# Kernel tuning notes

Measured on AMD Instinct MI355X. Metric: run time of the kernel, lower is better.

## Reference

```python
import jax, jax.numpy as jnp
import numpy as np

B, NLAT, NLON, V = 2, 181, 360, 78
NGRID = NLAT * NLON
NMESH, NEDGE = 10242, 163840
NODE_D, EDGE_D, HID, NLAYERS = 256, 64, 512, 16


def _mlp(x, w1, b1, w2, b2):
    # 2-layer MLP with ReLU (matches MLP(input_dim, hidden_dim, output_dim, n_layers=2))
    return jax.nn.relu(x @ w1 + b1) @ w2 + b2


def setup_inputs() -> dict:
    key = jax.random.key(0)
    ks = jax.random.split(key, 40)
    s = 0.02
    p = {}
    p["x_current"] = jax.random.normal(ks[0], (B, NLAT, NLON, V), jnp.float32)
    p["x_previous"] = jax.random.normal(ks[1], (B, NLAT, NLON, V), jnp.float32)
    p["mesh_node_feats"] = jax.random.normal(ks[2], (NMESH, 7), jnp.float32)
    p["raw_edge_feats"] = jax.random.normal(ks[3], (NEDGE, 4), jnp.float32)
    p["edge_index"] = jax.random.randint(ks[4], (2, NEDGE), 0, NMESH, jnp.int32)
    p["g2m_idx"] = jax.random.randint(ks[5], (NMESH,), 0, NGRID, jnp.int32)  # nearest grid point per mesh node
    p["m2g_idx"] = jax.random.randint(ks[6], (NGRID,), 0, NMESH, jnp.int32)  # nearest mesh node per grid point
    enc_in = 2 * V + 7  # grid channels (current||previous) + 7 mesh geometric features
    p["enc_w1"] = s * jax.random.normal(ks[7], (enc_in, HID), jnp.float32)
    p["enc_b1"] = jnp.zeros((HID,), jnp.float32)
    p["enc_w2"] = s * jax.random.normal(ks[8], (HID, NODE_D), jnp.float32)
    p["enc_b2"] = jnp.zeros((NODE_D,), jnp.float32)
    p["eme_w1"] = s * jax.random.normal(ks[9], (4, EDGE_D), jnp.float32)  # edge_embed: [dx,dy,dz,dist]->edge_dim
    p["eme_b1"] = jnp.zeros((EDGE_D,), jnp.float32)
    p["eme_w2"] = s * jax.random.normal(ks[10], (EDGE_D, EDGE_D), jnp.float32)
    p["eme_b2"] = jnp.zeros((EDGE_D,), jnp.float32)
    e_in = EDGE_D + 2 * NODE_D  # [edge, x_src, x_dst]
    n_in = NODE_D + EDGE_D      # [node, aggregated messages]
    p["pe_w1"] = s * jax.random.normal(ks[11], (NLAYERS, e_in, HID), jnp.float32)
    p["pe_b1"] = jnp.zeros((NLAYERS, HID), jnp.float32)
    p["pe_w2"] = s * jax.random.normal(ks[12], (NLAYERS, HID, EDGE_D), jnp.float32)
    p["pe_b2"] = jnp.zeros((NLAYERS, EDGE_D), jnp.float32)
    p["pn_w1"] = s * jax.random.normal(ks[13], (NLAYERS, n_in, HID), jnp.float32)
    p["pn_b1"] = jnp.zeros((NLAYERS, HID), jnp.float32)
    p["pn_w2"] = s * jax.random.normal(ks[14], (NLAYERS, HID, NODE_D), jnp.float32)
    p["pn_b2"] = jnp.zeros((NLAYERS, NODE_D), jnp.float32)
    p["dec_w1"] = s * jax.random.normal(ks[15], (NODE_D, HID), jnp.float32)
    p["dec_b1"] = jnp.zeros((HID,), jnp.float32)
    p["dec_w2"] = s * jax.random.normal(ks[16], (HID, V), jnp.float32)
    p["dec_b2"] = jnp.zeros((V,), jnp.float32)
    return p


def _forward(x_current, x_previous, mesh_node_feats, raw_edge_feats,
             enc_w1, enc_b1, enc_w2, enc_b2,
             eme_w1, eme_b1, eme_w2, eme_b2,
             pe_w1, pe_b1, pe_w2, pe_b2,
             pn_w1, pn_b1, pn_w2, pn_b2,
             dec_w1, dec_b1, dec_w2, dec_b2,
             edge_index, g2m_idx, m2g_idx):
    # --- Grid -> Mesh encoder ---
    x_input = jnp.concatenate([x_current, x_previous], axis=-1)           # (B, lat, lon, 2V)
    grid_flat = x_input.reshape(B, NGRID, 2 * V)
    gathered = grid_flat[:, g2m_idx]                                      # (B, NMESH, 2V)
    mesh_geo = jnp.broadcast_to(mesh_node_feats[None], (B, NMESH, 7))
    nodes = _mlp(jnp.concatenate([gathered, mesh_geo], -1),
                 enc_w1, enc_b1, enc_w2, enc_b2)                          # (B, NMESH, node_dim)

    # --- Edge embedding (shared initial edges) ---
    edges0 = _mlp(raw_edge_feats, eme_w1, eme_b1, eme_w2, eme_b2)         # (NEDGE, edge_dim)
    src, dst = edge_index[0], edge_index[1]

    def gnn_single(x):
        def layer(carry, params):
            x, e = carry
            w1e, b1e, w2e, b2e, w1n, b1n, w2n, b2n = params
            msg_in = jnp.concatenate([e, x[src], x[dst]], axis=-1)        # (NEDGE, edge+2*node)
            e = e + _mlp(msg_in, w1e, b1e, w2e, b2e)                      # residual edge update
            agg = jax.ops.segment_sum(e, dst, num_segments=NMESH)         # scatter-add to receivers
            x = x + _mlp(jnp.concatenate([x, agg], -1), w1n, b1n, w2n, b2n)
            return (x, e), None
        (x, _), _ = jax.lax.scan(layer, (x, edges0),
                                 (pe_w1, pe_b1, pe_w2, pe_b2, pn_w1, pn_b1, pn_w2, pn_b2))
        return x

    nodes = jax.vmap(gnn_single)(nodes)                                   # batch loop -> vmap

    # --- Mesh -> Grid decoder ---
    grid_nodes = nodes[:, m2g_idx]                                        # (B, NGRID, node_dim)
    delta = _mlp(grid_nodes, dec_w1, dec_b1, dec_w2, dec_b2)              # (B, NGRID, V)
    return delta.reshape(B, NLAT, NLON, V)


def reference(x_current, x_previous, mesh_node_feats, raw_edge_feats,
              enc_w1, enc_b1, enc_w2, enc_b2,
              eme_w1, eme_b1, eme_w2, eme_b2,
              pe_w1, pe_b1, pe_w2, pe_b2,
              pn_w1, pn_b1, pn_w2, pn_b2,
              dec_w1, dec_b1, dec_w2, dec_b2,
              edge_index, g2m_idx, m2g_idx):
    return _forward(x_current, x_previous, mesh_node_feats, raw_edge_feats,
                    enc_w1, enc_b1, enc_w2, enc_b2,
                    eme_w1, eme_b1, eme_w2, eme_b2,
                    pe_w1, pe_b1, pe_w2, pe_b2,
                    pn_w1, pn_b1, pn_w2, pn_b2,
                    dec_w1, dec_b1, dec_w2, dec_b2,
                    edge_index, g2m_idx, m2g_idx)
```

## Files before the change

### kernel.cpp

```cpp
#include <hip/hip_runtime.h>

#define P_NLAT  181
#define P_NLON  360
#define P_V     78
#define P_NGRID (P_NLAT * P_NLON)
#define P_B     2
#define P_NMESH 10242
#define P_NEDGE 163840
#define P_ND    256
#define P_ED    64
#define P_HID   512
#define P_NLAYERS 16

typedef __bf16 bf16x8 __attribute__((ext_vector_type(8)));
typedef unsigned short u16x8 __attribute__((ext_vector_type(8)));
typedef float f32x4 __attribute__((ext_vector_type(4)));

__device__ __forceinline__ unsigned short f2bf(float f) {
  union { float f; unsigned u; } x; x.f = f;
  unsigned r = x.u + 0x7FFFu + ((x.u >> 16) & 1u);
  return (unsigned short)(r >> 16);
}
__device__ __forceinline__ float bf2f(unsigned short h) {
  union { unsigned u; float f; } x; x.u = ((unsigned)h) << 16; return x.f;
}

__device__ __forceinline__ void gl_lds16(const unsigned short* gp, unsigned short* lp) {
  __builtin_amdgcn_global_load_lds(
      (const __attribute__((address_space(1))) unsigned int*)gp,
      (__attribute__((address_space(3))) unsigned int*)lp, 16, 0, 0);
}

struct GArgs {
  int amode;
  const unsigned short* A; long lda; long a_bstride;
  const int* gidx; int gr_off; int gr_per_b; int gsrc_rows_per_b;
  int M, K;
  const unsigned short* Wt;
  const float* bias; int Nreal; int relu;
  unsigned short* out16; long ldo16; long o16_bstride; long dup16;
  float* out32; long ldo32; long o32_bstride; long dup32;
  const float* resid; long r_bstride;
};

#define BM 128

template<int BN, int WM, int WN>
__global__ void __launch_bounds__(256) gemm_k(GArgs g) {
  constexpr int MI = WM / 16, NJ = WN / 16;
  constexpr int WPN = BN / WN;
  __shared__ unsigned short As[BM * 64];
  __shared__ unsigned short Bs[BN * 64];

  const int tid  = threadIdx.x;
  const int lane = tid & 63, wid = tid >> 6;
  const int wm = (wid / WPN) * WM, wn = (wid % WPN) * WN;
  const int bm = blockIdx.x * BM;
  const int bn = blockIdx.y * BN;
  const int z  = blockIdx.z;

  const unsigned short* Ad = g.A + (long)z * g.a_bstride;

  f32x4 acc[MI][NJ];
  #pragma unroll
  for (int i = 0; i < MI; ++i)
    #pragma unroll
    for (int j = 0; j < NJ; ++j) { f32x4 zv = {0.f, 0.f, 0.f, 0.f}; acc[i][j] = zv; }

  const int nKt = g.K >> 6;
  for (int kt = 0; kt < nKt; ++kt) {
    const int k0 = kt << 6;
    #pragma unroll
    for (int it = 0; it < (BM * 8) / 256; ++it) {
      int v = tid + it * 256;
      int r = v >> 3, j = v & 7;
      int row = bm + r; if (row >= g.M) row = g.M - 1;
      int kk = k0 + ((j ^ (r & 7)) << 3);
      const unsigned short* s;
      if (g.amode == 0) {
        s = Ad + (long)row * g.lda + kk;
      } else {
        int gr = g.gr_off + row;
        int b = gr / g.gr_per_b, loc = gr - b * g.gr_per_b;
        s = g.A + ((long)b * g.gsrc_rows_per_b + g.gidx[loc]) * g.lda + kk;
      }
      gl_lds16(s, &As[v << 3]);
    }
    #pragma unroll
    for (int it = 0; it < (BN * 8) / 256; ++it) {
      int v = tid + it * 256;
      int n = v >> 3, j = v & 7;
      gl_lds16(g.Wt + (long)(bn + n) * g.K + k0 + ((j ^ (n & 7)) << 3), &Bs[v << 3]);
    }
    __syncthreads();
    #pragma unroll
    for (int ko = 0; ko < 2; ++ko) {
      bf16x8 af[MI], bfr[NJ];
      #pragma unroll
      for (int i = 0; i < MI; ++i) {
        int ar = wm + i * 16 + (lane & 15);
        int ch = ((ko * 4 + (lane >> 4)) ^ (ar & 7)) << 3;
        u16x8 t = *(const u16x8*)&As[ar * 64 + ch];
        af[i] = __builtin_bit_cast(bf16x8, t);
      }
      #pragma unroll
      for (int j = 0; j < NJ; ++j) {
        int br = wn + j * 16 + (lane & 15);
        int ch = ((ko * 4 + (lane >> 4)) ^ (br & 7)) << 3;
        u16x8 t = *(const u16x8*)&Bs[br * 64 + ch];
        bfr[j] = __builtin_bit_cast(bf16x8, t);
      }
      #pragma unroll
      for (int i = 0; i < MI; ++i)
        #pragma unroll
        for (int j = 0; j < NJ; ++j)
          acc[i][j] = __builtin_amdgcn_mfma_f32_16x16x32_bf16(af[i], bfr[j], acc[i][j], 0, 0, 0);
    }
    __syncthreads();
  }

  unsigned short* o16 = g.out16 ? g.out16 + (long)z * g.o16_bstride : (unsigned short*)0;
  float* o32 = g.out32 ? g.out32 + (long)z * g.o32_bstride : (float*)0;
  const float* res = g.resid ? g.resid + (long)z * g.r_bstride : (const float*)0;
  const int q = lane >> 4, cc = lane & 15;
  #pragma unroll
  for (int i = 0; i < MI; ++i) {
    #pragma unroll
    for (int r = 0; r < 4; ++r) {
      int row = bm + wm + i * 16 + q * 4 + r;
      if (row >= g.M) continue;
      const float* rr = res ? res + (long)row * g.ldo32 : (const float*)0;
      #pragma unroll
      for (int j = 0; j < NJ; ++j) {
        int col = bn + wn + j * 16 + cc;
        if (col >= g.Nreal) continue;
        float v = acc[i][j][r];
        if (g.bias) v += g.bias[col];
        if (rr) v += rr[col];
        if (g.relu && v < 0.f) v = 0.f;
        if (o32) {
          long idx = (long)row * g.ldo32 + col;
          o32[idx] = v; if (g.dup32) o32[idx + g.dup32] = v;
        }
        if (o16) {
          long idx = (long)row * g.ldo16 + col;
          unsigned short h = f2bf(v);
          o16[idx] = h; if (g.dup16) o16[idx + g.dup16] = h;
        }
      }
    }
  }
}

struct FEArgs {
  unsigned short* E16;
  float* E32;
  const unsigned short* PSPD;
  const int* srcP; const int* dstP;
  const unsigned short* W1t;
  const unsigned short* W2t;
  const float* b1; const float* b2;
};

__global__ void __launch_bounds__(256, 4) fused_edge(FEArgs g) {
  __shared__ unsigned short As[64 * 64];
  __shared__ float HS[64 * 68];
  __shared__ unsigned short WS[64 * 64];

  const int tid = threadIdx.x, lane = tid & 63, wid = tid >> 6;
  const int q = lane >> 4, cc = lane & 15;
  const int z = blockIdx.y;
  const long gr0 = (long)blockIdx.x * 64;
  const long EB = (long)P_NEDGE * 64;
  unsigned short* E16z = g.E16 + z * EB;
  float* E32z = g.E32 + z * EB;
  const int moff = z * P_NMESH;
  unsigned short* HSb = (unsigned short*)HS;
  const int wm = wid * 16;

  #pragma unroll
  for (int it = 0; it < 2; ++it) {
    int v = tid + it * 256;
    int r = v >> 3, j = v & 7;
    gl_lds16(E16z + (gr0 + r) * 64 + ((j ^ (r & 7)) << 3), &As[v << 3]);
  }

  f32x4 acc2[4];
  #pragma unroll
  for (int j = 0; j < 4; ++j) { f32x4 zv = {0.f, 0.f, 0.f, 0.f}; acc2[j] = zv; }

  for (int hc = 0; hc < 8; ++hc) {
    #pragma unroll
    for (int it = 0; it < 2; ++it) {
      int v = tid + it * 256;
      int n = v >> 3, j = v & 7;
      gl_lds16(g.W1t + (long)(hc * 64 + n) * 64 + ((j ^ (n & 7)) << 3), &WS[v << 3]);
    }
    __syncthreads();

    f32x4 acc1[4];
    #pragma unroll
    for (int j = 0; j < 4; ++j) { f32x4 zv = {0.f, 0.f, 0.f, 0.f}; acc1[j] = zv; }
    #pragma unroll
    for (int ko = 0; ko < 2; ++ko) {
      int ar = wm + cc;
      u16x8 ta = *(const u16x8*)&As[ar * 64 + (((ko * 4 + q) ^ (ar & 7)) << 3)];
      bf16x8 af = __builtin_bit_cast(bf16x8, ta);
      #pragma unroll
      for (int j = 0; j < 4; ++j) {
        int n = j * 16 + cc;
        u16x8 tb = *(const u16x8*)&WS[n * 64 + (((ko * 4 + q) ^ (n & 7)) << 3)];
        bf16x8 bf = __builtin_bit_cast(bf16x8, tb);
        acc1[j] = __builtin_amdgcn_mfma_f32_16x16x32_bf16(af, bf, acc1[j], 0, 0, 0);
      }
    }
    #pragma unroll
    for (int j = 0; j < 4; ++j)
      #pragma unroll
      for (int r = 0; r < 4; ++r)
        HS[(wm + q * 4 + r) * 68 + j * 16 + cc] = acc1[j][r];
    __syncthreads();

    #pragma unroll
    for (int it = 0; it < 2; ++it) {
      int v = tid + it * 256;
      int n = v >> 3, j = v & 7;
      gl_lds16(g.W2t + (long)n * 512 + hc * 64 + ((j ^ (n & 7)) << 3), &WS[v << 3]);
    }
    float hv[2][8];
    #pragma unroll
    for (int it = 0; it < 2; ++it) {
      int v = tid + it * 256;
      int r = v >> 3, c8 = (v & 7) << 3;
      long grow = gr0 + r;
      const unsigned short* ps = g.PSPD + (long)(moff + g.srcP[grow]) * 1024 + hc * 64 + c8;
      const unsigned short* pd = g.PSPD + (long)(moff + g.dstP[grow]) * 1024 + 512 + hc * 64 + c8;
      u16x8 psv = *(const u16x8*)ps;
      u16x8 pdv = *(const u16x8*)pd;
      f32x4 ha = *(const f32x4*)&HS[r * 68 + c8];
      f32x4 hb = *(const f32x4*)&HS[r * 68 + c8 + 4];
      const float* b1p = g.b1 + hc * 64 + c8;
      #pragma unroll
      for (int e = 0; e < 8; ++e) {
        float x = (e < 4 ? ha[e] : hb[e - 4]) + b1p[e] + bf2f(psv[e]) + bf2f(pdv[e]);
        hv[it][e] = x < 0.f ? 0.f : x;
      }
    }
    __syncthreads();

    #pragma unroll
    for (int it = 0; it < 2; ++it) {
      int v = tid + it * 256;
      int r = v >> 3, j = v & 7;
      u16x8 outv;
      #pragma unroll
      for (int e = 0; e < 8; ++e) outv[e] = f2bf(hv[it][e]);
      *(u16x8*)&HSb[r * 64 + ((j ^ (r & 7)) << 3)] = outv;
    }
    __syncthreads();

    #pragma unroll
    for (int ko = 0; ko < 2; ++ko) {
      int ar = wm + cc;
      u16x8 ta = *(const u16x8*)&HSb[ar * 64 + (((ko * 4 + q) ^ (ar & 7)) << 3)];
      bf16x8 af = __builtin_bit_cast(bf16x8, ta);
      #pragma unroll
      for (int j = 0; j < 4; ++j) {
        int n = j * 16 + cc;
        u16x8 tb = *(const u16x8*)&WS[n * 64 + (((ko * 4 + q) ^ (n & 7)) << 3)];
        bf16x8 bf = __builtin_bit_cast(bf16x8, tb);
        acc2[j] = __builtin_amdgcn_mfma_f32_16x16x32_bf16(af, bf, acc2[j], 0, 0, 0);
      }
    }
    __syncthreads();
  }

  #pragma unroll
  for (int j = 0; j < 4; ++j) {
    #pragma unroll
    for (int r = 0; r < 4; ++r) {
      int row = wm + q * 4 + r;
      int col = j * 16 + cc;
      long idx = (gr0 + row) * 64 + col;
      float v = acc2[j][r] + g.b2[col] + E32z[idx];
      E32z[idx] = v;
      E16z[idx] = f2bf(v);
    }
  }
}

__global__ void wt_conv(const float* W, unsigned short* Wt, int K, int N, int Kpad, int Npad,
                        int row_off, long in_lstride, long out_lstride) {
  long t = (long)blockIdx.x * 256 + threadIdx.x;
  long tot = (long)Npad * Kpad;
  if (t >= tot) return;
  int n = (int)(t / Kpad), k = (int)(t - (long)n * Kpad);
  const float* Wl = W + (long)blockIdx.z * in_lstride + (long)row_off * N;
  float v = (n < N && k < K) ? Wl[(long)k * N + n] : 0.f;
  Wt[(long)blockIdx.z * out_lstride + t] = f2bf(v);
}

__global__ void build_enc_in(const float* xc, const float* xp, const float* mesh,
                             const int* g2m, unsigned short* out) {
  long t = (long)blockIdx.x * 256 + threadIdx.x;
  const long tot = (long)P_B * P_NMESH * 192;
  if (t >= tot) return;
  int k = (int)(t % 192); long r = t / 192;
  int m = (int)(r % P_NMESH); int b = (int)(r / P_NMESH);
  float v = 0.f;
  if (k < P_V)              v = xc[((long)b * P_NGRID + g2m[m]) * P_V + k];
  else if (k < 2 * P_V)     v = xp[((long)b * P_NGRID + g2m[m]) * P_V + (k - P_V)];
  else if (k < 2 * P_V + 7) v = mesh[m * 7 + (k - 2 * P_V)];
  out[t] = f2bf(v);
}

__global__ void build_rawpad(const float* raw, const int* perm, unsigned short* out) {
  long t = (long)blockIdx.x * 256 + threadIdx.x;
  const long tot = (long)P_NEDGE * 64;
  if (t >= tot) return;
  int k = (int)(t & 63); long r = t >> 6;
  int e = perm[r];
  out[t] = f2bf(k < 4 ? raw[(long)e * 4 + k] : 0.f);
}

__global__ void csr_hist(const int* dst, int* cnt) {
  int e = blockIdx.x * 256 + threadIdx.x;
  if (e < P_NEDGE) atomicAdd(&cnt[dst[e]], 1);
}
__global__ void csr_scan(const int* cnt, int* rowptr) {
  __shared__ int part[1024];
  int t = threadIdx.x;
  const int C = (P_NMESH + 1023) / 1024;
  int base = t * C, s = 0;
  for (int i = 0; i < C; ++i) { int idx = base + i; if (idx < P_NMESH) s += cnt[idx]; }
  part[t] = s; __syncthreads();
  for (int ofs = 1; ofs < 1024; ofs <<= 1) {
    int v = (t >= ofs) ? part[t - ofs] : 0;
    __syncthreads();
    part[t] += v;
    __syncthreads();
  }
  int excl = (t == 0) ? 0 : part[t - 1];
  for (int i = 0; i < C; ++i) {
    int idx = base + i;
    if (idx < P_NMESH) { rowptr[idx] = excl; excl += cnt[idx]; }
  }
  if (t == 1023) rowptr[P_NMESH] = excl;
}
__global__ void csr_scatter(const int* dst, const int* rowptr, int* cursor, int* perm) {
  int e = blockIdx.x * 256 + threadIdx.x;
  if (e < P_NEDGE) {
    int d = dst[e];
    int pos = atomicAdd(&cursor[d], 1);
    perm[rowptr[d] + pos] = e;
  }
}
__global__ void csr_permsd(const int* perm, const int* src, const int* dst, int* srcP, int* dstP) {
  int i = blockIdx.x * 256 + threadIdx.x;
  if (i < P_NEDGE) { int p = perm[i]; srcP[i] = src[p]; dstP[i] = dst[p]; }
}

__global__ void seg_reduce(const float* E32, const int* rowptr, unsigned short* XN) {
  int node = blockIdx.x * 4 + (threadIdx.x >> 6);
  int c = threadIdx.x & 63;
  int b = blockIdx.y;
  if (node >= P_NMESH) return;
  int r0 = rowptr[node], r1 = rowptr[node + 1];
  const float* base = E32 + (long)b * P_NEDGE * 64;
  float s = 0.f;
  for (int r = r0; r < r1; ++r) s += base[(long)r * 64 + c];
  XN[((long)b * P_NMESH + node) * 320 + 256 + c] = f2bf(s);
}

extern "C" void kernel_launch(void* const* d_in, const int* in_sizes, int n_in,
                              void* d_out, int out_size, void* d_ws, size_t ws_size,
                              hipStream_t stream) {
  (void)in_sizes; (void)n_in; (void)out_size;
  const float* x_current  = (const float*)d_in[0];
  const float* x_previous = (const float*)d_in[1];
  const float* mesh_feats = (const float*)d_in[2];
  const float* raw_edge   = (const float*)d_in[3];
  const int*   edge_index = (const int*)d_in[4];
  const int*   g2m        = (const int*)d_in[5];
  const int*   m2g        = (const int*)d_in[6];
  const float* enc_w1 = (const float*)d_in[7];
  const float* enc_b1 = (const float*)d_in[8];
  const float* enc_w2 = (const float*)d_in[9];
  const float* enc_b2 = (const float*)d_in[10];
  const float* eme_w1 = (const float*)d_in[11];
  const float* eme_b1 = (const float*)d_in[12];
  const float* eme_w2 = (const float*)d_in[13];
  const float* eme_b2 = (const float*)d_in[14];
  const float* pe_w1 = (const float*)d_in[15];
  const float* pe_b1 = (const float*)d_in[16];
  const float* pe_w2 = (const float*)d_in[17];
  const float* pe_b2 = (const float*)d_in[18];
  const float* pn_w1 = (const float*)d_in[19];
  const float* pn_b1 = (const float*)d_in[20];
  const float* pn_w2 = (const float*)d_in[21];
  const float* pn_b2 = (const float*)d_in[22];
  const float* dec_w1 = (const float*)d_in[23];
  const float* dec_b1 = (const float*)d_in[24];
  const float* dec_w2 = (const float*)d_in[25];
  const float* dec_b2 = (const float*)d_in[26];
  const int* srcI = edge_index;
  const int* dstI = edge_index + P_NEDGE;
  float* out = (float*)d_out;

  char* wsb = (char*)d_ws; size_t off = 0;
  auto alloc = [&](size_t bytes) -> void* {
    off = (off + 255) & ~(size_t)255;
    void* p = wsb + off; off += bytes; return p;
  };
  auto au16 = [&](long n) { return (unsigned short*)alloc((size_t)n * 2); };
  auto af32 = [&](long n) { return (float*)alloc((size_t)n * 4); };
  auto ai32 = [&](long n) { return (int*)alloc((size_t)n * 4); };

  unsigned short* enc_w1t   = au16(512L * 192);
  unsigned short* enc_w2t   = au16(256L * 512);
  unsigned short* eme_w1t   = au16(64L * 64);
  unsigned short* eme_w2t   = au16(64L * 64);
  unsigned short* pe_w1e_t  = au16(16L * 512 * 64);
  unsigned short* pe_w1sd_t = au16(16L * 1024 * 256);
  unsigned short* pe_w2t    = au16(16L * 64 * 512);
  unsigned short* pn_w1t    = au16(16L * 512 * 320);
  unsigned short* pn_w2t    = au16(16L * 256 * 512);
  unsigned short* dec_w1t   = au16(512L * 256);
  unsigned short* dec_w2t   = au16(128L * 512);
  int* cnt    = ai32(P_NMESH);
  int* cursor = ai32(P_NMESH);
  int* rowptr = ai32(P_NMESH + 1);
  int* perm   = ai32(P_NEDGE);
  int* srcP   = ai32(P_NEDGE);
  int* dstP   = ai32(P_NEDGE);
  float*          X32 = af32((long)P_B * P_NMESH * P_ND);
  unsigned short* XN  = au16((long)P_B * P_NMESH * 320);
  float*          E32 = af32((long)P_B * P_NEDGE * P_ED);
  unsigned short* E16 = au16((long)P_B * P_NEDGE * P_ED);
  size_t encin_b  = ((size_t)P_B * P_NMESH * 192 * 2 + 255) & ~(size_t)255;
  size_t rawpad_b = ((size_t)P_NEDGE * 64 * 2 + 255) & ~(size_t)255;
  size_t pspd_b   = ((size_t)P_B * P_NMESH * 1024 * 2 + 255) & ~(size_t)255;
  size_t reg1_b   = encin_b + rawpad_b; if (pspd_b > reg1_b) reg1_b = pspd_b;
  char* region1 = (char*)alloc(reg1_b);
  unsigned short* ENCIN  = (unsigned short*)region1;
  unsigned short* RAWPAD = (unsigned short*)(region1 + encin_b);
  unsigned short* PSPD   = (unsigned short*)region1;

  size_t rem = (ws_size > off + 4096) ? ws_size - off - 4096 : 0;
  size_t hb_full = (size_t)P_B * P_NGRID * 512 * 2;
  int DC; size_t hb;
  if (rem >= hb_full)          { DC = 1; hb = hb_full; }
  else if (rem >= hb_full / 2) { DC = 2; hb = hb_full / 2; }
  else                         { DC = 4; hb = hb_full / 4; }
  unsigned short* HBUF = (unsigned short*)alloc(hb);

  auto run128 = [&](const GArgs& a, int Npad, int zdim) {
    dim3 grid((a.M + BM - 1) / BM, Npad / 128, zdim);
    gemm_k<128, 64, 64><<<grid, dim3(256), 0, stream>>>(a);
  };
  auto run64 = [&](const GArgs& a, int zdim) {
    dim3 grid((a.M + BM - 1) / BM, 1, zdim);
    gemm_k<64, 32, 64><<<grid, dim3(256), 0, stream>>>(a);
  };
  auto convw = [&](const float* W, unsigned short* Wt, int K, int N, int Kp, int Np,
                   int row_off, long in_lst, long out_lst, int L) {
    long tot = (long)Np * Kp;
    wt_conv<<<dim3((unsigned)((tot + 255) / 256), 1, L), dim3(256), 0, stream>>>(
        W, Wt, K, N, Kp, Np, row_off, in_lst, out_lst);
  };

  hipMemsetAsync(cnt, 0, P_NMESH * 4, stream);
  hipMemsetAsync(cursor, 0, P_NMESH * 4, stream);
  csr_hist<<<dim3(P_NEDGE / 256), dim3(256), 0, stream>>>(dstI, cnt);
  csr_scan<<<dim3(1), dim3(1024), 0, stream>>>(cnt, rowptr);
  csr_scatter<<<dim3(P_NEDGE / 256), dim3(256), 0, stream>>>(dstI, rowptr, cursor, perm);
  csr_permsd<<<dim3(P_NEDGE / 256), dim3(256), 0, stream>>>(perm, srcI, dstI, srcP, dstP);

  convw(enc_w1, enc_w1t, 163, 512, 192, 512, 0, 163L * 512, 192L * 512, 1);
  convw(enc_w2, enc_w2t, 512, 256, 512, 256, 0, 512L * 256, 512L * 256, 1);
  convw(eme_w1, eme_w1t, 4, 64, 64, 64, 0, 4L * 64, 64L * 64, 1);
  convw(eme_w2, eme_w2t, 64, 64, 64, 64, 0, 64L * 64, 64L * 64, 1);
  convw(pe_w1, pe_w1e_t, 64, 512, 64, 512, 0, 576L * 512, 512L * 64, 16);
  convw(pe_w1, pe_w1sd_t, 256, 512, 256, 512, 64, 576L * 512, 1024L * 256, 16);
  convw(pe_w1, pe_w1sd_t + 512L * 256, 256, 512, 256, 512, 320, 576L * 512, 1024L * 256, 16);
  convw(pe_w2, pe_w2t, 512, 64, 512, 64, 0, 512L * 64, 64L * 512, 16);
  convw(pn_w1, pn_w1t, 320, 512, 320, 512, 0, 320L * 512, 512L * 320, 16);
  convw(pn_w2, pn_w2t, 512, 256, 512, 256, 0, 512L * 256, 256L * 512, 16);
  convw(dec_w1, dec_w1t, 256, 512, 256, 512, 0, 256L * 512, 512L * 256, 1);
  convw(dec_w2, dec_w2t, 512, 78, 512, 128, 0, 512L * 78, 128L * 512, 1);

  { long tot = (long)P_B * P_NMESH * 192;
    build_enc_in<<<dim3((unsigned)((tot + 255) / 256)), dim3(256), 0, stream>>>(
        x_current, x_previous, mesh_feats, g2m, ENCIN); }
  { long tot = (long)P_NEDGE * 64;
    build_rawpad<<<dim3((unsigned)((tot + 255) / 256)), dim3(256), 0, stream>>>(
        raw_edge, perm, RAWPAD); }

  { GArgs a{}; a.amode = 0; a.A = ENCIN; a.lda = 192; a.M = P_B * P_NMESH; a.K = 192;
    a.Wt = enc_w1t; a.bias = enc_b1; a.Nreal = 512; a.relu = 1;
    a.out16 = HBUF; a.ldo16 = 512; run128(a, 512, 1); }
  { GArgs a{}; a.amode = 0; a.A = HBUF; a.lda = 512; a.M = P_B * P_NMESH; a.K = 512;
    a.Wt = enc_w2t; a.bias = enc_b2; a.Nreal = 256; a.relu = 0;
    a.out32 = X32; a.ldo32 = 256; a.out16 = XN; a.ldo16 = 320; run128(a, 256, 1); }

  { GArgs a{}; a.amode = 0; a.A = RAWPAD; a.lda = 64; a.M = P_NEDGE; a.K = 64;
    a.Wt = eme_w1t; a.bias = eme_b1; a.Nreal = 64; a.relu = 1;
    a.out16 = HBUF; a.ldo16 = 64; run64(a, 1); }
  { GArgs a{}; a.amode = 0; a.A = HBUF; a.lda = 64; a.M = P_NEDGE; a.K = 64;
    a.Wt = eme_w2t; a.bias = eme_b2; a.Nreal = 64; a.relu = 0;
    a.out32 = E32; a.ldo32 = 64; a.dup32 = (long)P_NEDGE * 64;
    a.out16 = E16; a.ldo16 = 64; a.dup16 = (long)P_NEDGE * 64; run64(a, 1); }

  for (int l = 0; l < P_NLAYERS; ++l) {
    { GArgs a{}; a.amode = 0; a.A = XN; a.lda = 320; a.M = P_B * P_NMESH; a.K = 256;
      a.Wt = pe_w1sd_t + (long)l * 1024 * 256; a.Nreal = 1024; a.relu = 0;
      a.out16 = PSPD; a.ldo16 = 1024; run128(a, 1024, 1); }
    { FEArgs f{}; f.E16 = E16; f.E32 = E32; f.PSPD = PSPD;
      f.srcP = srcP; f.dstP = dstP;
      f.W1t = pe_w1e_t + (long)l * 512 * 64;
      f.W2t = pe_w2t + (long)l * 64 * 512;
      f.b1 = pe_b1 + l * 512; f.b2 = pe_b2 + l * 64;
      fused_edge<<<dim3(P_NEDGE / 64, P_B), dim3(256), 0, stream>>>(f); }
    seg_reduce<<<dim3((P_NMESH + 3) / 4, P_B), dim3(256), 0, stream>>>(E32, rowptr, XN);
    { GArgs a{}; a.amode = 0; a.A = XN; a.lda = 320; a.M = P_B * P_NMESH; a.K = 320;
      a.Wt = pn_w1t + (long)l * 512 * 320; a.bias = pn_b1 + l * 512; a.Nreal = 512; a.relu = 1;
      a.out16 = HBUF; a.ldo16 = 512; run128(a, 512, 1); }
    { GArgs a{}; a.amode = 0; a.A = HBUF; a.lda = 512; a.M = P_B * P_NMESH; a.K = 512;
      a.Wt = pn_w2t + (long)l * 256 * 512; a.bias = pn_b2 + l * 256; a.Nreal = 256; a.relu = 0;
      a.resid = X32; a.out32 = X32; a.ldo32 = 256; a.out16 = XN; a.ldo16 = 320;
      run128(a, 256, 1); }
  }

  const int dcrows = (P_B * P_NGRID) / DC;
  for (int c = 0; c < DC; ++c) {
    int c0 = c * dcrows;
    { GArgs a{}; a.amode = 2; a.A = XN; a.lda = 320;
      a.gidx = m2g; a.gr_off = c0; a.gr_per_b = P_NGRID; a.gsrc_rows_per_b = P_NMESH;
      a.M = dcrows; a.K = 256;
      a.Wt = dec_w1t; a.bias = dec_b1; a.Nreal = 512; a.relu = 1;
      a.out16 = HBUF; a.ldo16 = 512; run128(a, 512, 1); }
    { GArgs a{}; a.amode = 0; a.A = HBUF; a.lda = 512; a.M = dcrows; a.K = 512;
      a.Wt = dec_w2t; a.bias = dec_b2; a.Nreal = 78; a.relu = 0;
      a.out32 = out + (long)c0 * P_V; a.ldo32 = P_V;
      run128(a, 128, 1); }
  }
}
```

Baseline: 5.015 ms.

## Fuse edge-message aggregation into fused_edge via atomics and retile warps to 2x2

The fused edge kernel now does the scatter-sum of updated edge features itself. It stages outputs in LDS, run-length-sums contiguous destination rows (edges are CSR-sorted), and atomically adds the sums into an fp32 aggregate buffer. A small convert kernel then writes that buffer into XN as bf16 and zeroes it. This replaces the separate seg_reduce pass that re-read all E32. The warp tiling changes from 16x64 strips to 32x32 quadrants, and the hidden tile is stored in LDS as bf16 in place rather than fp32, which shrinks shared memory to 24KB and raises the occupancy hint to 6. The costs are atomic contention and summation order that is no longer deterministic.

```diff
diff --git a/kernel.cpp b/kernel.cpp
--- a/kernel.cpp
+++ b/kernel.cpp
@@ -160,12 +160,15 @@
   const unsigned short* W1t;
   const unsigned short* W2t;
   const float* b1; const float* b2;
+  float* AGG;
 };
 
-__global__ void __launch_bounds__(256, 4) fused_edge(FEArgs g) {
-  __shared__ unsigned short As[64 * 64];
-  __shared__ float HS[64 * 68];
-  __shared__ unsigned short WS[64 * 64];
+__global__ void __launch_bounds__(256, 6) fused_edge(FEArgs g) {
+  __shared__ char SMEM[24576];
+  unsigned short* As = (unsigned short*)SMEM;
+  unsigned short* HS = (unsigned short*)(SMEM + 8192);
+  unsigned short* WS = (unsigned short*)(SMEM + 16384);
+  float* LDSE = (float*)SMEM;
 
   const int tid = threadIdx.x, lane = tid & 63, wid = tid >> 6;
   const int q = lane >> 4, cc = lane & 15;
@@ -174,9 +177,9 @@
   const long EB = (long)P_NEDGE * 64;
   unsigned short* E16z = g.E16 + z * EB;
   float* E32z = g.E32 + z * EB;
+  float* AGGz = g.AGG + (long)z * P_NMESH * 64;
   const int moff = z * P_NMESH;
-  unsigned short* HSb = (unsigned short*)HS;
-  const int wm = wid * 16;
+  const int wm = (wid >> 1) * 32, wn = (wid & 1) * 32;
 
   #pragma unroll
   for (int it = 0; it < 2; ++it) {
@@ -185,11 +188,14 @@
     gl_lds16(E16z + (gr0 + r) * 64 + ((j ^ (r & 7)) << 3), &As[v << 3]);
   }
 
-  f32x4 acc2[4];
+  f32x4 acc2[2][2];
   #pragma unroll
-  for (int j = 0; j < 4; ++j) { f32x4 zv = {0.f, 0.f, 0.f, 0.f}; acc2[j] = zv; }
+  for (int i = 0; i < 2; ++i)
+    #pragma unroll
+    for (int j = 0; j < 2; ++j) { f32x4 zv = {0.f, 0.f, 0.f, 0.f}; acc2[i][j] = zv; }
 
   for (int hc = 0; hc < 8; ++hc) {
+    __syncthreads();
     #pragma unroll
     for (int it = 0; it < 2; ++it) {
       int v = tid + it * 256;
@@ -198,27 +204,42 @@
     }
     __syncthreads();
 
-    f32x4 acc1[4];
-    #pragma unroll
-    for (int j = 0; j < 4; ++j) { f32x4 zv = {0.f, 0.f, 0.f, 0.f}; acc1[j] = zv; }
+    f32x4 acc1[2][2];
+    #pragma unroll
+    for (int i = 0; i < 2; ++i)
+      #pragma unroll
+      for (int j = 0; j < 2; ++j) { f32x4 zv = {0.f, 0.f, 0.f, 0.f}; acc1[i][j] = zv; }
     #pragma unroll
     for (int ko = 0; ko < 2; ++ko) {
-      int ar = wm + cc;
-      u16x8 ta = *(const u16x8*)&As[ar * 64 + (((ko * 4 + q) ^ (ar & 7)) << 3)];
-      bf16x8 af = __builtin_bit_cast(bf16x8, ta);
-      #pragma unroll
-      for (int j = 0; j < 4; ++j) {
-        int n = j * 16 + cc;
-        u16x8 tb = *(const u16x8*)&WS[n * 64 + (((ko * 4 + q) ^ (n & 7)) << 3)];
-        bf16x8 bf = __builtin_bit_cast(bf16x8, tb);
-        acc1[j] = __builtin_amdgcn_mfma_f32_16x16x32_bf16(af, bf, acc1[j], 0, 0, 0);
-      }
-    }
-    #pragma unroll
-    for (int j = 0; j < 4; ++j)
-      #pragma unroll
-      for (int r = 0; r < 4; ++r)
-        HS[(wm + q * 4 + r) * 68 + j * 16 + cc] = acc1[j][r];
+      bf16x8 af[2], bfr[2];
+      #pragma unroll
+      for (int i = 0; i < 2; ++i) {
+        int ar = wm + i * 16 + cc;
+        u16x8 t = *(const u16x8*)&As[ar * 64 + (((ko * 4 + q) ^ (ar & 7)) << 3)];
+        af[i] = __builtin_bit_cast(bf16x8, t);
+      }
+      #pragma unroll
+      for (int j = 0; j < 2; ++j) {
+        int n = wn + j * 16 + cc;
+        u16x8 t = *(const u16x8*)&WS[n * 64 + (((ko * 4 + q) ^ (n & 7)) << 3)];
+        bfr[j] = __builtin_bit_cast(bf16x8, t);
+      }
+      #pragma unroll
+      for (int i = 0; i < 2; ++i)
+        #pragma unroll
+        for (int j = 0; j < 2; ++j)
+          acc1[i][j] = __builtin_amdgcn_mfma_f32_16x16x32_bf16(af[i], bfr[j], acc1[i][j], 0, 0, 0);
+    }
+    #pragma unroll
+    for (int i = 0; i < 2; ++i)
+      #pragma unroll
+      for (int j = 0; j < 2; ++j)
+        #pragma unroll
+        for (int r = 0; r < 4; ++r) {
+          int row = wm + i * 16 + q * 4 + r;
+          int col = wn + j * 16 + cc;
+          HS[row * 64 + ((((col >> 3) ^ (row & 7))) << 3) + (col & 7)] = f2bf(acc1[i][j][r]);
+        }
     __syncthreads();
 
     #pragma unroll
@@ -227,66 +248,92 @@
       int n = v >> 3, j = v & 7;
       gl_lds16(g.W2t + (long)n * 512 + hc * 64 + ((j ^ (n & 7)) << 3), &WS[v << 3]);
     }
-    float hv[2][8];
     #pragma unroll
     for (int it = 0; it < 2; ++it) {
       int v = tid + it * 256;
-      int r = v >> 3, c8 = (v & 7) << 3;
+      int r = v >> 3, jc = v & 7;
+      int c8 = jc << 3;
+      unsigned short* hp = &HS[r * 64 + ((jc ^ (r & 7)) << 3)];
+      u16x8 hraw = *(const u16x8*)hp;
       long grow = gr0 + r;
       const unsigned short* ps = g.PSPD + (long)(moff + g.srcP[grow]) * 1024 + hc * 64 + c8;
       const unsigned short* pd = g.PSPD + (long)(moff + g.dstP[grow]) * 1024 + 512 + hc * 64 + c8;
       u16x8 psv = *(const u16x8*)ps;
       u16x8 pdv = *(const u16x8*)pd;
-      f32x4 ha = *(const f32x4*)&HS[r * 68 + c8];
-      f32x4 hb = *(const f32x4*)&HS[r * 68 + c8 + 4];
       const float* b1p = g.b1 + hc * 64 + c8;
+      u16x8 outv;
       #pragma unroll
       for (int e = 0; e < 8; ++e) {
-        float x = (e < 4 ? ha[e] : hb[e - 4]) + b1p[e] + bf2f(psv[e]) + bf2f(pdv[e]);
-        hv[it][e] = x < 0.f ? 0.f : x;
-      }
-    }
-    __syncthreads();
-
-    #pragma unroll
-    for (int it = 0; it < 2; ++it) {
-      int v = tid + it * 256;
-      int r = v >> 3, j = v & 7;
-      u16x8 outv;
-      #pragma unroll
-      for (int e = 0; e < 8; ++e) outv[e] = f2bf(hv[it][e]);
-      *(u16x8*)&HSb[r * 64 + ((j ^ (r & 7)) << 3)] = outv;
+        float x = bf2f(hraw[e]) + b1p[e] + bf2f(psv[e]) + bf2f(pdv[e]);
+        outv[e] = f2bf(x < 0.f ? 0.f : x);
+      }
+      *(u16x8*)hp = outv;
     }
     __syncthreads();
 
     #pragma unroll
     for (int ko = 0; ko < 2; ++ko) {
-      int ar = wm + cc;
-      u16x8 ta = *(const u16x8*)&HSb[ar * 64 + (((ko * 4 + q) ^ (ar & 7)) << 3)];
-      bf16x8 af = __builtin_bit_cast(bf16x8, ta);
-      #pragma unroll
-      for (int j = 0; j < 4; ++j) {
-        int n = j * 16 + cc;
-        u16x8 tb = *(const u16x8*)&WS[n * 64 + (((ko * 4 + q) ^ (n & 7)) << 3)];
-        bf16x8 bf = __builtin_bit_cast(bf16x8, tb);
-        acc2[j] = __builtin_amdgcn_mfma_f32_16x16x32_bf16(af, bf, acc2[j], 0, 0, 0);
-      }
-    }
-    __syncthreads();
-  }
+      bf16x8 af[2], bfr[2];
+      #pragma unroll
+      for (int i = 0; i < 2; ++i) {
+        int ar = wm + i * 16 + cc;
+        u16x8 t = *(const u16x8*)&HS[ar * 64 + (((ko * 4 + q) ^ (ar & 7)) << 3)];
+        af[i] = __builtin_bit_cast(bf16x8, t);
+      }
+      #pragma unroll
+      for (int j = 0; j < 2; ++j) {
+        int n = wn + j * 16 + cc;
+        u16x8 t = *(const u16x8*)&WS[n * 64 + (((ko * 4 + q) ^ (n & 7)) << 3)];
+        bfr[j] = __builtin_bit_cast(bf16x8, t);
+      }
+      #pragma unroll
+      for (int i = 0; i < 2; ++i)
+        #pragma unroll
+        for (int j = 0; j < 2; ++j)
+          acc2[i][j] = __builtin_amdgcn_mfma_f32_16x16x32_bf16(af[i], bfr[j], acc2[i][j], 0, 0, 0);
+    }
+  }
+  __syncthreads();
 
   #pragma unroll
-  for (int j = 0; j < 4; ++j) {
-    #pragma unroll
-    for (int r = 0; r < 4; ++r) {
-      int row = wm + q * 4 + r;
-      int col = j * 16 + cc;
-      long idx = (gr0 + row) * 64 + col;
-      float v = acc2[j][r] + g.b2[col] + E32z[idx];
-      E32z[idx] = v;
-      E16z[idx] = f2bf(v);
-    }
-  }
+  for (int i = 0; i < 2; ++i)
+    #pragma unroll
+    for (int j = 0; j < 2; ++j)
+      #pragma unroll
+      for (int r = 0; r < 4; ++r) {
+        int row = wm + i * 16 + q * 4 + r;
+        int col = wn + j * 16 + cc;
+        long idx = (gr0 + row) * 64 + col;
+        float v = acc2[i][j][r] + g.b2[col] + E32z[idx];
+        E32z[idx] = v;
+        E16z[idx] = f2bf(v);
+        LDSE[row * 66 + col] = v;
+      }
+  __syncthreads();
+
+  {
+    int col = tid & 63;
+    int rbase = (tid >> 6) * 16;
+    int cur = g.dstP[gr0 + rbase];
+    float s = 0.f;
+    #pragma unroll
+    for (int r2 = 0; r2 < 16; ++r2) {
+      int d = g.dstP[gr0 + rbase + r2];
+      float v = LDSE[(rbase + r2) * 66 + col];
+      if (d != cur) { atomicAdd(&AGGz[(long)cur * 64 + col], s); cur = d; s = 0.f; }
+      s += v;
+    }
+    atomicAdd(&AGGz[(long)cur * 64 + col], s);
+  }
+}
+
+__global__ void convert_agg(float* AGG, unsigned short* XN) {
+  long t = (long)blockIdx.x * 256 + threadIdx.x;
+  const long tot = (long)P_B * P_NMESH * 64;
+  if (t >= tot) return;
+  int c = (int)(t & 63); long rn = t >> 6;
+  XN[rn * 320 + 256 + c] = f2bf(AGG[t]);
+  AGG[t] = 0.f;
 }
 
 __global__ void wt_conv(const float* W, unsigned short* Wt, int K, int N, int Kpad, int Npad,
@@ -358,18 +405,6 @@
 __global__ void csr_permsd(const int* perm, const int* src, const int* dst, int* srcP, int* dstP) {
   int i = blockIdx.x * 256 + threadIdx.x;
   if (i < P_NEDGE) { int p = perm[i]; srcP[i] = src[p]; dstP[i] = dst[p]; }
-}
-
-__global__ void seg_reduce(const float* E32, const int* rowptr, unsigned short* XN) {
-  int node = blockIdx.x * 4 + (threadIdx.x >> 6);
-  int c = threadIdx.x & 63;
-  int b = blockIdx.y;
-  if (node >= P_NMESH) return;
-  int r0 = rowptr[node], r1 = rowptr[node + 1];
-  const float* base = E32 + (long)b * P_NEDGE * 64;
-  float s = 0.f;
-  for (int r = r0; r < r1; ++r) s += base[(long)r * 64 + c];
-  XN[((long)b * P_NMESH + node) * 320 + 256 + c] = f2bf(s);
 }
 
 extern "C" void kernel_launch(void* const* d_in, const int* in_sizes, int n_in,
@@ -437,6 +472,7 @@
   unsigned short* XN  = au16((long)P_B * P_NMESH * 320);
   float*          E32 = af32((long)P_B * P_NEDGE * P_ED);
   unsigned short* E16 = au16((long)P_B * P_NEDGE * P_ED);
+  float*          AGG = af32((long)P_B * P_NMESH * 64);
   size_t encin_b  = ((size_t)P_B * P_NMESH * 192 * 2 + 255) & ~(size_t)255;
   size_t rawpad_b = ((size_t)P_NEDGE * 64 * 2 + 255) & ~(size_t)255;
   size_t pspd_b   = ((size_t)P_B * P_NMESH * 1024 * 2 + 255) & ~(size_t)255;
@@ -471,6 +507,7 @@
 
   hipMemsetAsync(cnt, 0, P_NMESH * 4, stream);
   hipMemsetAsync(cursor, 0, P_NMESH * 4, stream);
+  hipMemsetAsync(AGG, 0, (size_t)P_B * P_NMESH * 64 * 4, stream);
   csr_hist<<<dim3(P_NEDGE / 256), dim3(256), 0, stream>>>(dstI, cnt);
   csr_scan<<<dim3(1), dim3(1024), 0, stream>>>(cnt, rowptr);
   csr_scatter<<<dim3(P_NEDGE / 256), dim3(256), 0, stream>>>(dstI, rowptr, cursor, perm);
@@ -520,8 +557,10 @@
       f.W1t = pe_w1e_t + (long)l * 512 * 64;
       f.W2t = pe_w2t + (long)l * 64 * 512;
       f.b1 = pe_b1 + l * 512; f.b2 = pe_b2 + l * 64;
+      f.AGG = AGG;
       fused_edge<<<dim3(P_NEDGE / 64, P_B), dim3(256), 0, stream>>>(f); }
-    seg_reduce<<<dim3((P_NMESH + 3) / 4, P_B), dim3(256), 0, stream>>>(E32, rowptr, XN);
+    { long tot = (long)P_B * P_NMESH * 64;
+      convert_agg<<<dim3((unsigned)((tot + 255) / 256)), dim3(256), 0, stream>>>(AGG, XN); }
     { GArgs a{}; a.amode = 0; a.A = XN; a.lda = 320; a.M = P_B * P_NMESH; a.K = 320;
       a.Wt = pn_w1t + (long)l * 512 * 320; a.bias = pn_b1 + l * 512; a.Nreal = 512; a.relu = 1;
       a.out16 = HBUF; a.ldo16 = 512; run128(a, 512, 1); }
```

New measurement: 8.830 ms. +76.1%, slower.
